# Kernel tuning notes

Measured on AMD Instinct MI355X. Metric: run time of the kernel, lower is better.

The kernel has to match this reference:

```python
import jax, jax.numpy as jnp
import numpy as np

H, FF, E = 1024, 4096, 8
CAP_FACTOR, MIN_CAP = 1.0, 4
B, S = 4, 2048


def setup_inputs() -> dict:
    key = jax.random.key(0)
    ks = jax.random.split(key, 8)
    g = lambda k, shape, sc: jax.random.normal(k, shape, jnp.float32) * sc
    return {
        "hidden_states": jax.random.normal(ks[0], (B, S, H), jnp.float32),
        "wg": g(ks[1], (H, E), 0.02),
        "w1": g(ks[2], (E, H, FF), 0.02),
        "w2": g(ks[3], (E, FF, H), 0.02),
        "res_w1": g(ks[4], (H, FF), 0.02),
        "res_w2": g(ks[5], (FF, H), 0.02),
        "coef_w": g(ks[6], (H, 2), 0.02),
        "coef_b": jnp.zeros((2,), jnp.float32),
    }


def reference(hidden_states, wg, w1, w2, res_w1, res_w2, coef_w, coef_b):
    x = hidden_states
    b, s, d = x.shape
    tokens = x.reshape(-1, d)                      # [s, m] flattened tokens
    n = tokens.shape[0]
    capacity = max(MIN_CAP, int(CAP_FACTOR * n / E))  # static

    # ---- TopKGate (top-1, deterministic, no RTS) ----
    logits = tokens @ wg                            # [s, e]
    gates = jax.nn.softmax(logits, axis=1)
    idx1 = jnp.argmax(gates, axis=1)                # [s]
    mask1 = jax.nn.one_hot(idx1, E, dtype=jnp.int32)  # [s, e]
    exp_counts = mask1.sum(axis=0)                  # [e]
    # load-balancing aux loss (computed pre-capacity-drop, as in DeepSpeed)
    me = gates.mean(axis=0)
    ce = mask1.astype(gates.dtype).mean(axis=0)
    l_aux = jnp.sum(me * ce) * E
    # capacity-based token dropping (position within expert's buffer)
    locations1 = jnp.cumsum(mask1, axis=0) - 1      # [s, e]
    mask1 = mask1 * (locations1 < capacity).astype(jnp.int32)
    loc1_s = jnp.sum(locations1 * mask1, axis=1)    # [s]
    mask1f = mask1.astype(gates.dtype)
    gates_masked = gates * mask1f                   # zero except kept expert
    loc_sc = jax.nn.one_hot(loc1_s, capacity, dtype=gates.dtype)  # [s, c]
    combine = jnp.einsum("se,sc->sec", gates_masked, loc_sc)      # [s, e, c]
    dispatch = (combine > 0).astype(tokens.dtype)                 # [s, e, c]

    # ---- dispatch -> grouped expert FFN -> combine ----
    dispatched = jnp.einsum("sec,sm->ecm", dispatch, tokens)      # [e, c, m]
    h = jax.nn.gelu(jnp.einsum("ecm,emf->ecf", dispatched, w1))
    expert_out = jnp.einsum("ecf,efm->ecm", h, w2)                # [e, c, m]
    moe_out = jnp.einsum("sec,ecm->sm", combine, expert_out).reshape(b, s, d)

    # ---- residual MoE blend ----
    res = jax.nn.gelu(x @ res_w1) @ res_w2
    coef = jax.nn.softmax(x @ coef_w + coef_b, axis=-1)           # [b, s, 2]
    out = moe_out * coef[..., 0:1] + res * coef[..., 1:2]
    return out, l_aux, exp_counts
```

## Files before the change

### kernel.cpp

```cpp
#include <hip/hip_runtime.h>

typedef unsigned short u16;
typedef unsigned int u32;
typedef float f32x4 __attribute__((ext_vector_type(4)));
typedef __bf16 bf16x8 __attribute__((ext_vector_type(8)));

#define NTOK 8192
#define HDIM 1024
#define FFDIM 4096
#define NEXP 8
#define CAP 1024

typedef const __attribute__((address_space(1))) void gvoid_t;
typedef __attribute__((address_space(3))) void lvoid_t;

__device__ __forceinline__ u16 f2bf(float f) {
  u32 u = __float_as_uint(f);
  u += 0x7fffu + ((u >> 16) & 1u);
  return (u16)(u >> 16);
}

__device__ __forceinline__ float gelu_f(float x) {
  float u = 1.5957691216057308f * (x + 0.044715f * x * x * x);
  return x / (1.0f + __expf(-u));
}

__global__ __launch_bounds__(256) void convert_bf16(const float* __restrict__ src,
                                                    u16* __restrict__ dst,
                                                    long long n) {
  long long i = ((long long)blockIdx.x * 256 + threadIdx.x) * 8;
  if (i >= n) return;
  float4 f0 = *(const float4*)(src + i);
  float4 f1 = *(const float4*)(src + i + 4);
  union { u16 u[8]; uint4 v; } o;
  o.u[0] = f2bf(f0.x); o.u[1] = f2bf(f0.y); o.u[2] = f2bf(f0.z); o.u[3] = f2bf(f0.w);
  o.u[4] = f2bf(f1.x); o.u[5] = f2bf(f1.y); o.u[6] = f2bf(f1.z); o.u[7] = f2bf(f1.w);
  *(uint4*)(dst + i) = o.v;
}

__global__ __launch_bounds__(256) void transpose_f32_bf16(const float* __restrict__ src,
                                                          long long sBatch,
                                                          u16* __restrict__ dst,
                                                          long long dBatch,
                                                          int R, int C) {
  __shared__ float tile[32][33];
  int z = blockIdx.z;
  const float* s = src + (long long)z * sBatch;
  u16* d = dst + (long long)z * dBatch;
  int c0 = blockIdx.x * 32, r0 = blockIdx.y * 32;
  int tx = threadIdx.x, ty = threadIdx.y;
#pragma unroll
  for (int i = 0; i < 32; i += 8)
    tile[ty + i][tx] = s[(long long)(r0 + ty + i) * C + c0 + tx];
  __syncthreads();
#pragma unroll
  for (int i = 0; i < 32; i += 8)
    d[(long long)(c0 + ty + i) * R + r0 + tx] = f2bf(tile[tx][ty + i]);
}

__global__ __launch_bounds__(256) void gate_kernel(const float* __restrict__ x,
                                                   const float* __restrict__ wg,
                                                   const float* __restrict__ cw,
                                                   const float* __restrict__ cb,
                                                   int* __restrict__ idx1,
                                                   float* __restrict__ gate_val,
                                                   float* __restrict__ gates8,
                                                   float* __restrict__ coef) {
  const int wave = threadIdx.x >> 6, lane = threadIdx.x & 63;
  const int s = blockIdx.x * 4 + wave;
  const float* xr = x + (long long)s * HDIM;
  double p[10];
#pragma unroll
  for (int v = 0; v < 10; ++v) p[v] = 0.0;
#pragma unroll 4
  for (int i = 0; i < HDIM / 64; ++i) {
    int hh = i * 64 + lane;
    float xv = xr[hh];
    float4 w0 = *(const float4*)(wg + hh * 8);
    float4 w1 = *(const float4*)(wg + hh * 8 + 4);
    float2 c = *(const float2*)(cw + hh * 2);
    double xd = (double)xv;
    p[0] += xd * (double)w0.x; p[1] += xd * (double)w0.y;
    p[2] += xd * (double)w0.z; p[3] += xd * (double)w0.w;
    p[4] += xd * (double)w1.x; p[5] += xd * (double)w1.y;
    p[6] += xd * (double)w1.z; p[7] += xd * (double)w1.w;
    p[8] += xd * (double)c.x;  p[9] += xd * (double)c.y;
  }
#pragma unroll
  for (int v = 0; v < 10; ++v)
#pragma unroll
    for (int off = 32; off > 0; off >>= 1) p[v] += __shfl_down(p[v], off);
  if (lane == 0) {
    double mx = p[0]; int am = 0;
#pragma unroll
    for (int e = 1; e < 8; ++e)
      if (p[e] > mx) { mx = p[e]; am = e; }
    float g[8]; float sum = 0.f;
#pragma unroll
    for (int e = 0; e < 8; ++e) { g[e] = __expf((float)(p[e] - mx)); sum += g[e]; }
    float inv = 1.f / sum;
#pragma unroll
    for (int e = 0; e < 8; ++e) { g[e] *= inv; gates8[s * 8 + e] = g[e]; }
    idx1[s] = am;
    gate_val[s] = g[am];
    float c0 = (float)p[8] + cb[0], c1 = (float)p[9] + cb[1];
    float m2 = fmaxf(c0, c1);
    float e0 = __expf(c0 - m2), e1 = __expf(c1 - m2);
    float is = 1.f / (e0 + e1);
    coef[2 * s] = e0 * is;
    coef[2 * s + 1] = e1 * is;
  }
}

__global__ void scan_kernel(const int* __restrict__ idx1,
                            const float* __restrict__ gates8,
                            int* __restrict__ rowmap,
                            float* __restrict__ out_tail)
{
  int lane = threadIdx.x;
  int cnt[8];
  float me[8];
#pragma unroll
  for (int e = 0; e < 8; ++e) { cnt[e] = 0; me[e] = 0.f; }
  unsigned long long below = (lane == 0) ? 0ull : ((~0ull) >> (64 - lane));
  for (int it = 0; it < NTOK / 64; ++it) {
    int tok = it * 64 + lane;
    int e = idx1[tok];
    const float* g = gates8 + tok * 8;
#pragma unroll
    for (int xx = 0; xx < 8; ++xx) me[xx] += g[xx];
#pragma unroll
    for (int xx = 0; xx < 8; ++xx) {
      unsigned long long m = __ballot(e == xx);
      if (e == xx) {
        int pos = cnt[xx] + __popcll(m & below);
        if (pos < CAP) rowmap[xx * CAP + pos] = tok;
      }
      cnt[xx] += __popcll(m);
    }
  }
#pragma unroll
  for (int xx = 0; xx < 8; ++xx)
#pragma unroll
    for (int off = 32; off > 0; off >>= 1) me[xx] += __shfl_down(me[xx], off);
  if (lane == 0) {
    float laux = 0.f;
#pragma unroll
    for (int e = 0; e < 8; ++e) {
      out_tail[1 + e] = (float)cnt[e];
      laux += (me[e] / (float)NTOK) * ((float)cnt[e] / (float)NTOK);
    }
    out_tail[0] = laux * (float)NEXP;
  }
}

__global__ __launch_bounds__(256) void gemm128(
    const u16* __restrict__ Aall, long long aBatch,
    const u16* __restrict__ Ball, long long bBatch,
    int M, int N, int K,
    const int* __restrict__ amapAll,
    int mode,
    u16* __restrict__ hOut, long long hBatch,
    const int* __restrict__ rmapAll,
    const float* __restrict__ gate_val,
    float* __restrict__ moe_acc,
    const float* __restrict__ coef,
    float* __restrict__ outf) {
  const int z = blockIdx.z;
  const u16* A = Aall + (long long)z * aBatch;
  const u16* Bt = Ball + (long long)z * bBatch;

  const int tid = threadIdx.x;
  const int lane = tid & 63;
  const int wave = tid >> 6;
  const int wr = wave >> 1, wc = wave & 1;
  const int tileM = blockIdx.y * 128;
  const int tileN = blockIdx.x * 128;

  __shared__ __align__(16) u16 As[128 * 32];
  __shared__ __align__(16) u16 Bs[128 * 32];

  const int sr0 = wave * 32 + (lane >> 2);
  const int sr1 = sr0 + 16;
  const int cS = (lane & 3) << 3;

  long long gaA0, gaA1;
  if (amapAll) {
    const int* amap = amapAll + (long long)z * M;
    int s0 = amap[tileM + sr0]; gaA0 = s0 < 0 ? 0 : s0;
    int s1 = amap[tileM + sr1]; gaA1 = s1 < 0 ? 0 : s1;
  } else {
    gaA0 = tileM + sr0;
    gaA1 = tileM + sr1;
  }

  const u16* aG0 = A + gaA0 * K + cS;
  const u16* aG1 = A + gaA1 * K + cS;
  const u16* bG0 = Bt + (long long)(tileN + sr0) * K + cS;
  const u16* bG1 = Bt + (long long)(tileN + sr1) * K + cS;

  u16* asD0 = As + wave * 1024;
  u16* asD1 = As + wave * 1024 + 512;
  u16* bsD0 = Bs + wave * 1024;
  u16* bsD1 = Bs + wave * 1024 + 512;

  f32x4 acc[4][4];
  const f32x4 fz = {0.f, 0.f, 0.f, 0.f};
#pragma unroll
  for (int i = 0; i < 4; ++i)
#pragma unroll
    for (int j = 0; j < 4; ++j) acc[i][j] = fz;

  const int k8 = (lane >> 4) << 3;
  const int rlo = lane & 15;
  const u16* aRd = &As[(wr * 64 + rlo) * 32 + k8];
  const u16* bRd = &Bs[(wc * 64 + rlo) * 32 + k8];

  for (int kk = 0; kk < K; kk += 32) {
    __syncthreads();
    __builtin_amdgcn_global_load_lds((gvoid_t*)aG0, (lvoid_t*)asD0, 16, 0, 0);
    __builtin_amdgcn_global_load_lds((gvoid_t*)aG1, (lvoid_t*)asD1, 16, 0, 0);
    __builtin_amdgcn_global_load_lds((gvoid_t*)bG0, (lvoid_t*)bsD0, 16, 0, 0);
    __builtin_amdgcn_global_load_lds((gvoid_t*)bG1, (lvoid_t*)bsD1, 16, 0, 0);
    aG0 += 32; aG1 += 32; bG0 += 32; bG1 += 32;
    __syncthreads();
    bf16x8 af[4], bfr[4];
#pragma unroll
    for (int i = 0; i < 4; ++i) af[i] = *(const bf16x8*)(aRd + i * 16 * 32);
#pragma unroll
    for (int j = 0; j < 4; ++j) bfr[j] = *(const bf16x8*)(bRd + j * 16 * 32);
#pragma unroll
    for (int i = 0; i < 4; ++i)
#pragma unroll
      for (int j = 0; j < 4; ++j)
        acc[i][j] = __builtin_amdgcn_mfma_f32_16x16x32_bf16(af[i], bfr[j], acc[i][j], 0, 0, 0);
  }

  const int qr = (lane >> 4) * 4;
  const int cc = lane & 15;
  if (mode == 0) {
    u16* hO = hOut + (long long)z * hBatch;
#pragma unroll
    for (int i = 0; i < 4; ++i) {
      int rbase = tileM + wr * 64 + i * 16 + qr;
#pragma unroll
      for (int j = 0; j < 4; ++j) {
        int col = tileN + wc * 64 + j * 16 + cc;
#pragma unroll
        for (int r = 0; r < 4; ++r)
          hO[(long long)(rbase + r) * N + col] = f2bf(gelu_f(acc[i][j][r]));
      }
    }
  } else if (mode == 1) {
    const int* rmap = rmapAll + (long long)z * M;
#pragma unroll
    for (int i = 0; i < 4; ++i) {
      int rbase = tileM + wr * 64 + i * 16 + qr;
#pragma unroll
      for (int j = 0; j < 4; ++j) {
        int col = tileN + wc * 64 + j * 16 + cc;
#pragma unroll
        for (int r = 0; r < 4; ++r) {
          int s = rmap[rbase + r];
          if (s >= 0) moe_acc[(long long)s * HDIM + col] = gate_val[s] * acc[i][j][r];
        }
      }
    }
  } else {
#pragma unroll
    for (int i = 0; i < 4; ++i) {
      int rbase = tileM + wr * 64 + i * 16 + qr;
#pragma unroll
      for (int j = 0; j < 4; ++j) {
        int col = tileN + wc * 64 + j * 16 + cc;
#pragma unroll
        for (int r = 0; r < 4; ++r) {
          int s = rbase + r;
          outf[(long long)s * HDIM + col] =
              coef[2 * s] * moe_acc[(long long)s * HDIM + col] + coef[2 * s + 1] * acc[i][j][r];
        }
      }
    }
  }
}

extern "C" void kernel_launch(void* const* d_in, const int* in_sizes, int n_in,
                              void* d_out, int out_size, void* d_ws, size_t ws_size,
                              hipStream_t stream) {
  (void)in_sizes; (void)n_in; (void)out_size; (void)ws_size;
  const float* x   = (const float*)d_in[0];
  const float* wg  = (const float*)d_in[1];
  const float* w1  = (const float*)d_in[2];
  const float* w2  = (const float*)d_in[3];
  const float* rw1 = (const float*)d_in[4];
  const float* rw2 = (const float*)d_in[5];
  const float* cw  = (const float*)d_in[6];
  const float* cb  = (const float*)d_in[7];
  float* out = (float*)d_out;

  char* ws = (char*)d_ws;
  constexpr size_t OFF_XB   = 0;
  constexpr size_t OFF_W1T  = OFF_XB  + (size_t)NTOK * HDIM * 2;
  constexpr size_t OFF_W2T  = OFF_W1T + (size_t)NEXP * FFDIM * HDIM * 2;
  constexpr size_t OFF_H    = OFF_W2T + (size_t)NEXP * HDIM * FFDIM * 2;
  constexpr size_t OFF_MOE  = OFF_H   + (size_t)NEXP * CAP * FFDIM * 2;
  constexpr size_t OFF_GATE = OFF_MOE + (size_t)NTOK * HDIM * 4;
  constexpr size_t OFF_COEF = OFF_GATE + (size_t)NTOK * 4;
  constexpr size_t OFF_IDX  = OFF_COEF + (size_t)NTOK * 8;
  constexpr size_t OFF_RMAP = OFF_IDX + (size_t)NTOK * 4;
  constexpr size_t OFF_G8   = OFF_RMAP + (size_t)NEXP * CAP * 4;

  u16* xb        = (u16*)(ws + OFF_XB);
  u16* w1t       = (u16*)(ws + OFF_W1T);
  u16* w2t       = (u16*)(ws + OFF_W2T);
  u16* h         = (u16*)(ws + OFF_H);
  float* moe_acc = (float*)(ws + OFF_MOE);
  float* gate_v  = (float*)(ws + OFF_GATE);
  float* coef    = (float*)(ws + OFF_COEF);
  int* idx1      = (int*)(ws + OFF_IDX);
  int* rowmap    = (int*)(ws + OFF_RMAP);
  float* gates8  = (float*)(ws + OFF_G8);

  hipMemsetAsync(rowmap, 0xFF, (size_t)NEXP * CAP * 4, stream);
  hipMemsetAsync(moe_acc, 0, (size_t)NTOK * HDIM * 4, stream);

  convert_bf16<<<4096, 256, 0, stream>>>(x, xb, (long long)NTOK * HDIM);
  gate_kernel<<<NTOK / 4, 256, 0, stream>>>(x, wg, cw, cb, idx1, gate_v, gates8, coef);
  scan_kernel<<<1, 64, 0, stream>>>(idx1, gates8, rowmap, out + (size_t)NTOK * HDIM);

  transpose_f32_bf16<<<dim3(FFDIM / 32, HDIM / 32, NEXP), dim3(32, 8), 0, stream>>>(
      w1, (long long)HDIM * FFDIM, w1t, (long long)FFDIM * HDIM, HDIM, FFDIM);
  transpose_f32_bf16<<<dim3(HDIM / 32, FFDIM / 32, NEXP), dim3(32, 8), 0, stream>>>(
      w2, (long long)FFDIM * HDIM, w2t, (long long)HDIM * FFDIM, FFDIM, HDIM);

  gemm128<<<dim3(FFDIM / 128, CAP / 128, NEXP), 256, 0, stream>>>(
      xb, 0, w1t, (long long)FFDIM * HDIM, CAP, FFDIM, HDIM,
      rowmap, 0, h, (long long)CAP * FFDIM, nullptr, nullptr, nullptr, nullptr, nullptr);
  gemm128<<<dim3(HDIM / 128, CAP / 128, NEXP), 256, 0, stream>>>(
      h, (long long)CAP * FFDIM, w2t, (long long)HDIM * FFDIM, CAP, HDIM, FFDIM,
      nullptr, 1, nullptr, 0, rowmap, gate_v, moe_acc, nullptr, nullptr);

  transpose_f32_bf16<<<dim3(FFDIM / 32, HDIM / 32, 1), dim3(32, 8), 0, stream>>>(
      rw1, 0, w1t, 0, HDIM, FFDIM);
  transpose_f32_bf16<<<dim3(HDIM / 32, FFDIM / 32, 1), dim3(32, 8), 0, stream>>>(
      rw2, 0, w2t, 0, FFDIM, HDIM);

  gemm128<<<dim3(FFDIM / 128, NTOK / 128, 1), 256, 0, stream>>>(
      xb, 0, w1t, 0, NTOK, FFDIM, HDIM,
      nullptr, 0, h, 0, nullptr, nullptr, nullptr, nullptr, nullptr);
  gemm128<<<dim3(HDIM / 128, NTOK / 128, 1), 256, 0, stream>>>(
      h, 0, w2t, 0, NTOK, HDIM, FFDIM,
      nullptr, 2, nullptr, 0, nullptr, nullptr, moe_acc, coef, out);
}
```

Measured before the change: 1.015 ms.

## Double-buffer LDS tiles in the GEMM and XOR-swizzle the K chunks

The shared GEMM kernel now keeps two LDS buffers for the A and B tiles. It issues the global-to-LDS loads for the next K step before running the MFMAs on the current one, which drops one barrier per iteration and overlaps memory latency with compute. The 8-element K chunks are also XOR-swizzled by row, on both the global source column and the LDS read offset, to reduce LDS bank conflicts on the fragment reads. This doubles LDS use per block, which may lower occupancy, and correctness relies on the barrier waiting for the outstanding async loads.

After: 976.3 us. 1.04x faster.

```diff
diff --git a/kernel.cpp b/kernel.cpp
--- a/kernel.cpp
+++ b/kernel.cpp
@@ -177,12 +177,12 @@
   const int tileM = blockIdx.y * 128;
   const int tileN = blockIdx.x * 128;
 
-  __shared__ __align__(16) u16 As[128 * 32];
-  __shared__ __align__(16) u16 Bs[128 * 32];
+  __shared__ __align__(16) u16 As[2][128 * 32];
+  __shared__ __align__(16) u16 Bs[2][128 * 32];
 
   const int sr0 = wave * 32 + (lane >> 2);
   const int sr1 = sr0 + 16;
-  const int cS = (lane & 3) << 3;
+  const int cS = (((lane & 3) ^ ((lane >> 3) & 3)) << 3);
 
   long long gaA0, gaA1;
   if (amapAll) {
@@ -199,10 +199,7 @@
   const u16* bG0 = Bt + (long long)(tileN + sr0) * K + cS;
   const u16* bG1 = Bt + (long long)(tileN + sr1) * K + cS;
 
-  u16* asD0 = As + wave * 1024;
-  u16* asD1 = As + wave * 1024 + 512;
-  u16* bsD0 = Bs + wave * 1024;
-  u16* bsD1 = Bs + wave * 1024 + 512;
+  const int ldsChunk = wave * 1024;
 
   f32x4 acc[4][4];
   const f32x4 fz = {0.f, 0.f, 0.f, 0.f};
@@ -211,29 +208,40 @@
 #pragma unroll
     for (int j = 0; j < 4; ++j) acc[i][j] = fz;
 
-  const int k8 = (lane >> 4) << 3;
   const int rlo = lane & 15;
-  const u16* aRd = &As[(wr * 64 + rlo) * 32 + k8];
-  const u16* bRd = &Bs[(wc * 64 + rlo) * 32 + k8];
-
+  const int kq = lane >> 4;
+  const int swzR = (rlo >> 1) & 3;
+  const int aOff = (wr * 64 + rlo) * 32 + ((kq ^ swzR) << 3);
+  const int bOff = (wc * 64 + rlo) * 32 + ((kq ^ swzR) << 3);
+
+  __builtin_amdgcn_global_load_lds((gvoid_t*)aG0, (lvoid_t*)&As[0][ldsChunk], 16, 0, 0);
+  __builtin_amdgcn_global_load_lds((gvoid_t*)aG1, (lvoid_t*)&As[0][ldsChunk + 512], 16, 0, 0);
+  __builtin_amdgcn_global_load_lds((gvoid_t*)bG0, (lvoid_t*)&Bs[0][ldsChunk], 16, 0, 0);
+  __builtin_amdgcn_global_load_lds((gvoid_t*)bG1, (lvoid_t*)&Bs[0][ldsChunk + 512], 16, 0, 0);
+  aG0 += 32; aG1 += 32; bG0 += 32; bG1 += 32;
+
+  int cur = 0;
   for (int kk = 0; kk < K; kk += 32) {
     __syncthreads();
-    __builtin_amdgcn_global_load_lds((gvoid_t*)aG0, (lvoid_t*)asD0, 16, 0, 0);
-    __builtin_amdgcn_global_load_lds((gvoid_t*)aG1, (lvoid_t*)asD1, 16, 0, 0);
-    __builtin_amdgcn_global_load_lds((gvoid_t*)bG0, (lvoid_t*)bsD0, 16, 0, 0);
-    __builtin_amdgcn_global_load_lds((gvoid_t*)bG1, (lvoid_t*)bsD1, 16, 0, 0);
-    aG0 += 32; aG1 += 32; bG0 += 32; bG1 += 32;
-    __syncthreads();
+    if (kk + 32 < K) {
+      int nxt = cur ^ 1;
+      __builtin_amdgcn_global_load_lds((gvoid_t*)aG0, (lvoid_t*)&As[nxt][ldsChunk], 16, 0, 0);
+      __builtin_amdgcn_global_load_lds((gvoid_t*)aG1, (lvoid_t*)&As[nxt][ldsChunk + 512], 16, 0, 0);
+      __builtin_amdgcn_global_load_lds((gvoid_t*)bG0, (lvoid_t*)&Bs[nxt][ldsChunk], 16, 0, 0);
+      __builtin_amdgcn_global_load_lds((gvoid_t*)bG1, (lvoid_t*)&Bs[nxt][ldsChunk + 512], 16, 0, 0);
+      aG0 += 32; aG1 += 32; bG0 += 32; bG1 += 32;
+    }
     bf16x8 af[4], bfr[4];
 #pragma unroll
-    for (int i = 0; i < 4; ++i) af[i] = *(const bf16x8*)(aRd + i * 16 * 32);
-#pragma unroll
-    for (int j = 0; j < 4; ++j) bfr[j] = *(const bf16x8*)(bRd + j * 16 * 32);
+    for (int i = 0; i < 4; ++i) af[i] = *(const bf16x8*)(&As[cur][aOff + i * 16 * 32]);
+#pragma unroll
+    for (int j = 0; j < 4; ++j) bfr[j] = *(const bf16x8*)(&Bs[cur][bOff + j * 16 * 32]);
 #pragma unroll
     for (int i = 0; i < 4; ++i)
 #pragma unroll
       for (int j = 0; j < 4; ++j)
         acc[i][j] = __builtin_amdgcn_mfma_f32_16x16x32_bf16(af[i], bfr[j], acc[i][j], 0, 0, 0);
+    cur ^= 1;
   }
 
   const int qr = (lane >> 4) * 4;
```

## Double GEMM K-tile to 64 with XOR-swizzled LDS layout; prefetch scan loads

Applied to the files above, without the earlier changes.

The bf16 GEMM now stages a 64-wide K slice per iteration instead of 32. This halves the number of barrier pairs and global-to-LDS rounds per output tile. The LDS layout gets an XOR swizzle on 16-byte chunks so the MFMA fragment reads avoid bank conflicts. The scan kernel also prefetches the next iteration's expert index and gate values as float4 loads, at the cost of more LDS per block and somewhat higher register pressure.

Measured after the change: 898.0 us. -11.5%, faster.

```diff
diff --git a/kernel.cpp b/kernel.cpp
--- a/kernel.cpp
+++ b/kernel.cpp
@@ -123,12 +123,20 @@
 #pragma unroll
   for (int e = 0; e < 8; ++e) { cnt[e] = 0; me[e] = 0.f; }
   unsigned long long below = (lane == 0) ? 0ull : ((~0ull) >> (64 - lane));
+  int eN = idx1[lane];
+  float4 gN0 = *(const float4*)(gates8 + lane * 8);
+  float4 gN1 = *(const float4*)(gates8 + lane * 8 + 4);
   for (int it = 0; it < NTOK / 64; ++it) {
     int tok = it * 64 + lane;
-    int e = idx1[tok];
-    const float* g = gates8 + tok * 8;
-#pragma unroll
-    for (int xx = 0; xx < 8; ++xx) me[xx] += g[xx];
+    int e = eN;
+    float4 g0 = gN0, g1 = gN1;
+    if (it + 1 < NTOK / 64) {
+      eN = idx1[tok + 64];
+      gN0 = *(const float4*)(gates8 + (tok + 64) * 8);
+      gN1 = *(const float4*)(gates8 + (tok + 64) * 8 + 4);
+    }
+    me[0] += g0.x; me[1] += g0.y; me[2] += g0.z; me[3] += g0.w;
+    me[4] += g1.x; me[5] += g1.y; me[6] += g1.z; me[7] += g1.w;
 #pragma unroll
     for (int xx = 0; xx < 8; ++xx) {
       unsigned long long m = __ballot(e == xx);
@@ -177,32 +185,36 @@
   const int tileM = blockIdx.y * 128;
   const int tileN = blockIdx.x * 128;
 
-  __shared__ __align__(16) u16 As[128 * 32];
-  __shared__ __align__(16) u16 Bs[128 * 32];
-
-  const int sr0 = wave * 32 + (lane >> 2);
-  const int sr1 = sr0 + 16;
-  const int cS = (lane & 3) << 3;
-
-  long long gaA0, gaA1;
+  __shared__ __align__(16) u16 As[128 * 64];
+  __shared__ __align__(16) u16 Bs[128 * 64];
+
+  const int lrow = lane >> 3;
+  const int gk = (((lane & 7) ^ lrow) << 3);
+
+  int sr[4];
+#pragma unroll
+  for (int c = 0; c < 4; ++c) sr[c] = wave * 32 + c * 8 + lrow;
+
+  long long gaA[4];
   if (amapAll) {
     const int* amap = amapAll + (long long)z * M;
-    int s0 = amap[tileM + sr0]; gaA0 = s0 < 0 ? 0 : s0;
-    int s1 = amap[tileM + sr1]; gaA1 = s1 < 0 ? 0 : s1;
+#pragma unroll
+    for (int c = 0; c < 4; ++c) {
+      int s0 = amap[tileM + sr[c]];
+      gaA[c] = s0 < 0 ? 0 : s0;
+    }
   } else {
-    gaA0 = tileM + sr0;
-    gaA1 = tileM + sr1;
-  }
-
-  const u16* aG0 = A + gaA0 * K + cS;
-  const u16* aG1 = A + gaA1 * K + cS;
-  const u16* bG0 = Bt + (long long)(tileN + sr0) * K + cS;
-  const u16* bG1 = Bt + (long long)(tileN + sr1) * K + cS;
-
-  u16* asD0 = As + wave * 1024;
-  u16* asD1 = As + wave * 1024 + 512;
-  u16* bsD0 = Bs + wave * 1024;
-  u16* bsD1 = Bs + wave * 1024 + 512;
+#pragma unroll
+    for (int c = 0; c < 4; ++c) gaA[c] = tileM + sr[c];
+  }
+
+  const u16* aG[4];
+  const u16* bG[4];
+#pragma unroll
+  for (int c = 0; c < 4; ++c) {
+    aG[c] = A + gaA[c] * K + gk;
+    bG[c] = Bt + (long long)(tileN + sr[c]) * K + gk;
+  }
 
   f32x4 acc[4][4];
   const f32x4 fz = {0.f, 0.f, 0.f, 0.f};
@@ -211,29 +223,44 @@
 #pragma unroll
     for (int j = 0; j < 4; ++j) acc[i][j] = fz;
 
-  const int k8 = (lane >> 4) << 3;
   const int rlo = lane & 15;
-  const u16* aRd = &As[(wr * 64 + rlo) * 32 + k8];
-  const u16* bRd = &Bs[(wc * 64 + rlo) * 32 + k8];
-
-  for (int kk = 0; kk < K; kk += 32) {
+  const int kq = lane >> 4;
+  const int sw = rlo & 7;
+  const int ks0 = (kq ^ sw) << 3;
+  const int ks1 = ((4 | kq) ^ sw) << 3;
+  int aRow[4], bRow[4];
+#pragma unroll
+  for (int i = 0; i < 4; ++i) {
+    aRow[i] = (wr * 64 + i * 16 + rlo) * 64;
+    bRow[i] = (wc * 64 + i * 16 + rlo) * 64;
+  }
+
+  for (int kk = 0; kk < K; kk += 64) {
     __syncthreads();
-    __builtin_amdgcn_global_load_lds((gvoid_t*)aG0, (lvoid_t*)asD0, 16, 0, 0);
-    __builtin_amdgcn_global_load_lds((gvoid_t*)aG1, (lvoid_t*)asD1, 16, 0, 0);
-    __builtin_amdgcn_global_load_lds((gvoid_t*)bG0, (lvoid_t*)bsD0, 16, 0, 0);
-    __builtin_amdgcn_global_load_lds((gvoid_t*)bG1, (lvoid_t*)bsD1, 16, 0, 0);
-    aG0 += 32; aG1 += 32; bG0 += 32; bG1 += 32;
+#pragma unroll
+    for (int c = 0; c < 4; ++c) {
+      __builtin_amdgcn_global_load_lds((gvoid_t*)aG[c],
+          (lvoid_t*)&As[(wave * 32 + c * 8) * 64], 16, 0, 0);
+      __builtin_amdgcn_global_load_lds((gvoid_t*)bG[c],
+          (lvoid_t*)&Bs[(wave * 32 + c * 8) * 64], 16, 0, 0);
+      aG[c] += 64;
+      bG[c] += 64;
+    }
     __syncthreads();
-    bf16x8 af[4], bfr[4];
-#pragma unroll
-    for (int i = 0; i < 4; ++i) af[i] = *(const bf16x8*)(aRd + i * 16 * 32);
-#pragma unroll
-    for (int j = 0; j < 4; ++j) bfr[j] = *(const bf16x8*)(bRd + j * 16 * 32);
-#pragma unroll
-    for (int i = 0; i < 4; ++i)
-#pragma unroll
-      for (int j = 0; j < 4; ++j)
-        acc[i][j] = __builtin_amdgcn_mfma_f32_16x16x32_bf16(af[i], bfr[j], acc[i][j], 0, 0, 0);
+#pragma unroll
+    for (int sub = 0; sub < 2; ++sub) {
+      const int ks = sub ? ks1 : ks0;
+      bf16x8 af[4], bfr[4];
+#pragma unroll
+      for (int i = 0; i < 4; ++i) af[i] = *(const bf16x8*)(&As[aRow[i] + ks]);
+#pragma unroll
+      for (int j = 0; j < 4; ++j) bfr[j] = *(const bf16x8*)(&Bs[bRow[j] + ks]);
+#pragma unroll
+      for (int i = 0; i < 4; ++i)
+#pragma unroll
+        for (int j = 0; j < 4; ++j)
+          acc[i][j] = __builtin_amdgcn_mfma_f32_16x16x32_bf16(af[i], bfr[j], acc[i][j], 0, 0, 0);
+    }
   }
 
   const int qr = (lane >> 4) * 4;
```
